# Performance work log

Hardware: AMD Instinct MI355X
Metric: run time of the kernel (lower is better)

The kernel has to match this reference:

```python
import jax, jax.numpy as jnp
import numpy as np

B, C, H, W = 4, 32, 64, 64
D_STATE, D_CONV = 16, 4


def _mamba(x, Win, convw, convb, Wx, Wdt, dtb, Alog, D, Wout, dt_rank):
    Bsz, L, _ = x.shape
    d_in, K = convw.shape
    xz = x @ Win.T                                  # (B, L, 2*d_inner)
    xc, z = xz[..., :d_in], xz[..., d_in:]
    xp = jnp.pad(xc, ((0, 0), (K - 1, 0), (0, 0)))  # causal left pad
    xconv = convb + sum(convw[:, k] * xp[:, k:k + L, :] for k in range(K))
    xa = jax.nn.silu(xconv)                         # (B, L, d_inner)
    xdbl = xa @ Wx.T                                # (B, L, dt_rank + 2*N)
    dt = jax.nn.softplus(xdbl[..., :dt_rank] @ Wdt.T + dtb)     # (B, L, d_inner)
    Bm = xdbl[..., dt_rank:dt_rank + D_STATE]                   # (B, L, N)
    Cm = xdbl[..., dt_rank + D_STATE:]                          # (B, L, N)
    A = -jnp.exp(Alog)                                          # (d_inner, N)
    dA = jnp.exp(dt[..., None] * A)                             # (B, L, d_inner, N)
    dBu = dt[..., None] * Bm[:, :, None, :] * xa[..., None]     # (B, L, d_inner, N)

    def step(h, inp):
        dA_t, dBu_t, C_t = inp
        h = dA_t * h + dBu_t
        return h, jnp.einsum('bdn,bn->bd', h, C_t)

    h0 = jnp.zeros((Bsz, d_in, D_STATE), x.dtype)
    _, ys = jax.lax.scan(step, h0, (dA.transpose(1, 0, 2, 3), dBu.transpose(1, 0, 2, 3), Cm.transpose(1, 0, 2)))
    y = ys.transpose(1, 0, 2) + D * xa
    return (y * jax.nn.silu(z)) @ Wout.T


def _line_seqs(x):
    # x: (B,C,H,W) -> four (B, H*W, C) directional scan orders
    hf = x.reshape(B, C, H * W).transpose(0, 2, 1)
    hb = hf[:, ::-1, :]
    wf = x.transpose(0, 1, 3, 2).reshape(B, C, H * W).transpose(0, 2, 1)
    wb = wf[:, ::-1, :]
    return hf, hb, wf, wb


def _oss(fo1, fo2, p1, p2):
    hf, hb, wf, wb = _line_seqs(fo1)
    fop = jnp.concatenate([hf, hb, wf, wb], axis=2)       # (B, HW, 4C)
    fop = _mamba(fop, *p1, dt_rank=8)
    fop = fop.reshape(B, H * W, 4, C).sum(2)              # (B, HW, C)
    fop = fop.transpose(0, 2, 1).reshape(B, C, H, W)
    residual = fop * fo2
    foc = residual.mean(axis=(2, 3)).reshape(B, C, 1)     # adaptive_avg_pool2d (1,1)
    foc = jnp.concatenate([foc, foc[:, ::-1, :]], axis=2) # (B, C, 2)
    foc = _mamba(foc, *p2, dt_rank=1)
    foc = foc.sum(2, keepdims=True)[..., None]            # (B, C, 1, 1)
    return foc * residual + residual


def setup_inputs() -> dict:
    key = jax.random.key(0)
    ks = jax.random.split(key, 18)
    def n(k, shape, s=0.02):
        return jax.random.normal(k, shape, jnp.float32) * s
    dm1, di1, dr1 = 4 * C, 8 * C, 8
    dm2, di2, dr2 = 2, 4, 1
    return {
        'fo1': jax.random.normal(ks[0], (B, C, H, W), jnp.float32),
        'fo2': jax.random.normal(ks[1], (B, C, H, W), jnp.float32),
        'm1_Win': n(ks[2], (2 * di1, dm1)),
        'm1_convw': n(ks[3], (di1, D_CONV), 0.2),
        'm1_convb': n(ks[4], (di1,), 0.1),
        'm1_Wx': n(ks[5], (dr1 + 2 * D_STATE, di1)),
        'm1_Wdt': n(ks[6], (di1, dr1), 0.1),
        'm1_dtb': n(ks[7], (di1,), 0.5),
        'm1_Alog': jnp.log(jnp.tile(jnp.arange(1, D_STATE + 1, dtype=jnp.float32), (di1, 1))),
        'm1_D': jnp.ones((di1,), jnp.float32),
        'm1_Wout': n(ks[8], (dm1, di1)),
        'm2_Win': n(ks[9], (2 * di2, dm2)),
        'm2_convw': n(ks[10], (di2, D_CONV), 0.2),
        'm2_convb': n(ks[11], (di2,), 0.1),
        'm2_Wx': n(ks[12], (dr2 + 2 * D_STATE, di2)),
        'm2_Wdt': n(ks[13], (di2, dr2), 0.1),
        'm2_dtb': n(ks[14], (di2,), 0.5),
        'm2_Alog': jnp.log(jnp.tile(jnp.arange(1, D_STATE + 1, dtype=jnp.float32), (di2, 1))),
        'm2_D': jnp.ones((di2,), jnp.float32),
        'm2_Wout': n(ks[15], (dm2, di2)),
    }


def reference(fo1, fo2, m1_Win, m1_convw, m1_convb, m1_Wx, m1_Wdt, m1_dtb, m1_Alog, m1_D, m1_Wout,
              m2_Win, m2_convw, m2_convb, m2_Wx, m2_Wdt, m2_dtb, m2_Alog, m2_D, m2_Wout):
    p1 = (m1_Win, m1_convw, m1_convb, m1_Wx, m1_Wdt, m1_dtb, m1_Alog, m1_D, m1_Wout)
    p2 = (m2_Win, m2_convw, m2_convb, m2_Wx, m2_Wdt, m2_dtb, m2_Alog, m2_D, m2_Wout)
    return _oss(fo1, fo2, p1, p2)
```

## Files before the change

kernel.cpp:

```cpp
#include <hip/hip_runtime.h>
#include <cstddef>


typedef __attribute__((ext_vector_type(8))) short short8v;
typedef __attribute__((ext_vector_type(4))) float f32x4;

__device__ __forceinline__ float siluf(float x) { return x / (1.f + __expf(-x)); }
__device__ __forceinline__ float softplusf(float x) { return (x > 20.f) ? x : log1pf(__expf(x)); }
__device__ __forceinline__ unsigned short f2bf(float f) {
  union { float f; unsigned int u; } v; v.f = f;
  unsigned int r = v.u + 0x7fff + ((v.u >> 16) & 1);
  return (unsigned short)(r >> 16);
}
__device__ __forceinline__ float bf2f(unsigned short u) {
  union { unsigned int i; float f; } v; v.i = ((unsigned int)u) << 16; return v.f;
}

__global__ __launch_bounds__(256) void k_build_fop(const float* __restrict__ fo1,
                                                   unsigned short* __restrict__ fopb) {
  int idx = blockIdx.x * 256 + threadIdx.x;
  int j = idx & 127;
  int l = (idx >> 7) & 4095;
  int b = idx >> 19;
  int g = j >> 5, c = j & 31;
  const float* base = fo1 + (size_t)(b * 32 + c) * 4096;
  int li;
  if (g == 0)      li = l;
  else if (g == 1) li = 4095 - l;
  else if (g == 2) li = ((l & 63) << 6) + (l >> 6);
  else { int i2 = 4095 - l; li = ((i2 & 63) << 6) + (i2 >> 6); }
  fopb[idx] = f2bf(base[li]);
}

__global__ __launch_bounds__(256) void k_gemm1_mfma(const unsigned short* __restrict__ A,
                                                    const float* __restrict__ Win,
                                                    unsigned short* __restrict__ xcb,
                                                    float* __restrict__ zbuf) {
  __shared__ unsigned short As[128][136];
  __shared__ unsigned short Bs[64][136];
  int t = threadIdx.x;
  int bm = blockIdx.x * 128, bn = blockIdx.y * 64;
#pragma unroll
  for (int it = 0; it < 8; ++it) {
    int idx = t + it * 256;
    int r = idx >> 4, kc = idx & 15;
    short8v v = *(const short8v*)&A[(size_t)(bm + r) * 128 + kc * 8];
    *(short8v*)&As[r][kc * 8] = v;
  }
#pragma unroll
  for (int it = 0; it < 8; ++it) {
    int idx = t + it * 256;
    int r = idx >> 5, kq = idx & 31;
    float4 w = *(const float4*)&Win[(size_t)(bn + r) * 128 + kq * 4];
    ushort4 h;
    h.x = f2bf(w.x); h.y = f2bf(w.y); h.z = f2bf(w.z); h.w = f2bf(w.w);
    *(ushort4*)&Bs[r][kq * 4] = h;
  }
  __syncthreads();
  int lane = t & 63, w = t >> 6;
  int wm = (w & 1) * 64, wn = (w >> 1) * 32;
  int lr = lane & 15, lg = lane >> 4;
  f32x4 acc[4][2] = {};
#pragma unroll
  for (int k0 = 0; k0 < 128; k0 += 32) {
    short8v a[4], b[2];
#pragma unroll
    for (int mf = 0; mf < 4; ++mf)
      a[mf] = *(const short8v*)&As[wm + mf * 16 + lr][k0 + lg * 8];
#pragma unroll
    for (int nf = 0; nf < 2; ++nf)
      b[nf] = *(const short8v*)&Bs[wn + nf * 16 + lr][k0 + lg * 8];
#pragma unroll
    for (int mf = 0; mf < 4; ++mf)
#pragma unroll
      for (int nf = 0; nf < 2; ++nf)
        acc[mf][nf] = __builtin_amdgcn_mfma_f32_16x16x32_bf16(a[mf], b[nf], acc[mf][nf], 0, 0, 0);
  }
  if (bn < 256) {
#pragma unroll
    for (int mf = 0; mf < 4; ++mf)
#pragma unroll
      for (int nf = 0; nf < 2; ++nf)
#pragma unroll
        for (int r = 0; r < 4; ++r) {
          size_t row = bm + wm + mf * 16 + lg * 4 + r;
          xcb[row * 256 + bn + wn + nf * 16 + lr] = f2bf(acc[mf][nf][r]);
        }
  } else {
#pragma unroll
    for (int mf = 0; mf < 4; ++mf)
#pragma unroll
      for (int nf = 0; nf < 2; ++nf)
#pragma unroll
        for (int r = 0; r < 4; ++r) {
          size_t row = bm + wm + mf * 16 + lg * 4 + r;
          zbuf[row * 256 + (bn - 256) + wn + nf * 16 + lr] = acc[mf][nf][r];
        }
  }
}

__global__ __launch_bounds__(256) void k_gemm_nt(const float* __restrict__ A,
                                                 const float* __restrict__ W,
                                                 float* __restrict__ C,
                                                 int M, int N, int K, int lda) {
  __shared__ float As[32][68];
  __shared__ float Ws[32][68];
  int tid = threadIdx.x;
  int bm = blockIdx.x * 64;
  int bn = blockIdx.y * 64;
  int tx = tid & 15, ty = tid >> 4;
  float acc[4][4] = {};
  for (int k0 = 0; k0 < K; k0 += 32) {
#pragma unroll
    for (int it = 0; it < 2; ++it) {
      int idx = tid + it * 256;
      int r = idx >> 3;
      int kq = idx & 7;
      float4 v = *(const float4*)&A[(size_t)(bm + r) * lda + k0 + kq * 4];
      As[kq * 4 + 0][r] = v.x; As[kq * 4 + 1][r] = v.y;
      As[kq * 4 + 2][r] = v.z; As[kq * 4 + 3][r] = v.w;
      int n = bn + r;
      float4 w = make_float4(0.f, 0.f, 0.f, 0.f);
      if (n < N) w = *(const float4*)&W[(size_t)n * K + k0 + kq * 4];
      Ws[kq * 4 + 0][r] = w.x; Ws[kq * 4 + 1][r] = w.y;
      Ws[kq * 4 + 2][r] = w.z; Ws[kq * 4 + 3][r] = w.w;
    }
    __syncthreads();
#pragma unroll
    for (int k = 0; k < 32; ++k) {
      float4 a = *(const float4*)&As[k][ty * 4];
      float4 w = *(const float4*)&Ws[k][tx * 4];
      float av[4] = {a.x, a.y, a.z, a.w};
      float wv[4] = {w.x, w.y, w.z, w.w};
#pragma unroll
      for (int i = 0; i < 4; ++i)
#pragma unroll
        for (int j = 0; j < 4; ++j)
          acc[i][j] = fmaf(av[i], wv[j], acc[i][j]);
    }
    __syncthreads();
  }
#pragma unroll
  for (int i = 0; i < 4; ++i) {
    size_t m = bm + ty * 4 + i;
#pragma unroll
    for (int j = 0; j < 4; ++j) {
      int n = bn + tx * 4 + j;
      if (n < N) C[m * N + n] = acc[i][j];
    }
  }
}

__global__ __launch_bounds__(256) void k_conv_silu(const unsigned short* __restrict__ xcb,
                                                   const float* __restrict__ convw,
                                                   const float* __restrict__ convb,
                                                   float* __restrict__ xa) {
  int row = blockIdx.x;
  int l = row & 4095;
  int d = threadIdx.x;
  float4 w = *(const float4*)&convw[d * 4];
  float acc = convb[d];
  const unsigned short* p = xcb + (size_t)row * 256 + d;
  if (l >= 3) acc = fmaf(w.x, bf2f(p[-3 * 256]), acc);
  if (l >= 2) acc = fmaf(w.y, bf2f(p[-2 * 256]), acc);
  if (l >= 1) acc = fmaf(w.z, bf2f(p[-1 * 256]), acc);
  acc = fmaf(w.w, bf2f(p[0]), acc);
  xa[(size_t)row * 256 + d] = siluf(acc);
}

__global__ __launch_bounds__(256) void k_scan_p1(const float* __restrict__ xa,
                                                 const float* __restrict__ xdbl,
                                                 const float* __restrict__ Wdt,
                                                 const float* __restrict__ dtb,
                                                 const float* __restrict__ Alog,
                                                 float* __restrict__ Pb,
                                                 float* __restrict__ Qb) {
  __shared__ f32x4 xrow[32][10];
  __shared__ float xas[32][256];
  int t = threadIdx.x;
  int blk = blockIdx.x;
  int ch = blk & 127, b = blk >> 7;
  size_t row0 = (size_t)b * 4096 + ch * 32;
  for (int i = t; i < 320; i += 256) {
    int s = i / 10, q = i - s * 10;
    xrow[s][q] = *(const f32x4*)&xdbl[(row0 + s) * 40 + q * 4];
  }
#pragma unroll
  for (int it = 0; it < 8; ++it) {
    int i = t + it * 256;
    int s = i >> 6, q = i & 63;
    *(f32x4*)&xas[s][q * 4] = *(const f32x4*)&xa[(row0 + s) * 256 + q * 4];
  }
  __syncthreads();
  int d = t;
  f32x4 w0 = *(const f32x4*)&Wdt[d * 8];
  f32x4 w1 = *(const f32x4*)&Wdt[d * 8 + 4];
  float bias = dtb[d];
  float A[16], P[16], Q[16];
#pragma unroll
  for (int g = 0; g < 4; ++g) {
    f32x4 al = *(const f32x4*)&Alog[d * 16 + g * 4];
#pragma unroll
    for (int j = 0; j < 4; ++j) {
      A[g * 4 + j] = -__expf(al[j]);
      P[g * 4 + j] = 1.f;
      Q[g * 4 + j] = 0.f;
    }
  }
#pragma unroll 2
  for (int s = 0; s < 32; ++s) {
    f32x4 x0 = xrow[s][0], x1 = xrow[s][1];
    float v = bias;
#pragma unroll
    for (int j = 0; j < 4; ++j) v = fmaf(x0[j], w0[j], v);
#pragma unroll
    for (int j = 0; j < 4; ++j) v = fmaf(x1[j], w1[j], v);
    float ex = __expf(v);
    float dtv = (v > 20.f) ? v : __logf(1.f + ex);
    float du = dtv * xas[s][d];
    f32x4 bm[4];
#pragma unroll
    for (int g = 0; g < 4; ++g) bm[g] = xrow[s][2 + g];
#pragma unroll
    for (int n = 0; n < 16; ++n) {
      float e = __expf(dtv * A[n]);
      Q[n] = fmaf(e, Q[n], du * bm[n >> 2][n & 3]);
      P[n] *= e;
    }
  }
  size_t ob = (size_t)ch * 16384 + b * 4096 + d * 16;
#pragma unroll
  for (int g = 0; g < 4; ++g) {
    *(f32x4*)&Pb[ob + g * 4] = *(f32x4*)&P[g * 4];
    *(f32x4*)&Qb[ob + g * 4] = *(f32x4*)&Q[g * 4];
  }
}

__global__ __launch_bounds__(256) void k_scan_p2(const float* __restrict__ Pb,
                                                 const float* __restrict__ Qb,
                                                 float* __restrict__ Hin) {
  int t = blockIdx.x * 256 + threadIdx.x;
  float h = 0.f;
  size_t o = t;
#pragma unroll 8
  for (int ch = 0; ch < 128; ++ch) {
    Hin[o] = h;
    h = fmaf(Pb[o], h, Qb[o]);
    o += 16384;
  }
}

__global__ __launch_bounds__(256) void k_scan_p3(const float* __restrict__ xa,
                                                 const float* __restrict__ xdbl,
                                                 const float* __restrict__ Wdt,
                                                 const float* __restrict__ dtb,
                                                 const float* __restrict__ Alog,
                                                 const float* __restrict__ Hin,
                                                 const float* __restrict__ Dp,
                                                 const float* __restrict__ zbuf,
                                                 unsigned short* __restrict__ ym) {
  __shared__ f32x4 xrow[32][10];
  __shared__ float xas[32][256];
  int t = threadIdx.x;
  int blk = blockIdx.x;
  int ch = blk & 127, b = blk >> 7;
  size_t row0 = (size_t)b * 4096 + ch * 32;
  for (int i = t; i < 320; i += 256) {
    int s = i / 10, q = i - s * 10;
    xrow[s][q] = *(const f32x4*)&xdbl[(row0 + s) * 40 + q * 4];
  }
#pragma unroll
  for (int it = 0; it < 8; ++it) {
    int i = t + it * 256;
    int s = i >> 6, q = i & 63;
    *(f32x4*)&xas[s][q * 4] = *(const f32x4*)&xa[(row0 + s) * 256 + q * 4];
  }
  __syncthreads();
  int d = t;
  f32x4 w0 = *(const f32x4*)&Wdt[d * 8];
  f32x4 w1 = *(const f32x4*)&Wdt[d * 8 + 4];
  float bias = dtb[d];
  float Dd = Dp[d];
  float A[16], h[16];
  size_t hb = (size_t)ch * 16384 + b * 4096 + d * 16;
#pragma unroll
  for (int g = 0; g < 4; ++g) {
    f32x4 al = *(const f32x4*)&Alog[d * 16 + g * 4];
    f32x4 hv = *(const f32x4*)&Hin[hb + g * 4];
#pragma unroll
    for (int j = 0; j < 4; ++j) {
      A[g * 4 + j] = -__expf(al[j]);
      h[g * 4 + j] = hv[j];
    }
  }
  const float* zp = zbuf + row0 * 256 + d;
  unsigned short* yo = ym + row0 * 256 + d;
#pragma unroll 2
  for (int s = 0; s < 32; ++s) {
    f32x4 x0 = xrow[s][0], x1 = xrow[s][1];
    float v = bias;
#pragma unroll
    for (int j = 0; j < 4; ++j) v = fmaf(x0[j], w0[j], v);
#pragma unroll
    for (int j = 0; j < 4; ++j) v = fmaf(x1[j], w1[j], v);
    float ex = __expf(v);
    float dtv = (v > 20.f) ? v : __logf(1.f + ex);
    float xav = xas[s][d];
    float du = dtv * xav;
    f32x4 bm[4], cm[4];
#pragma unroll
    for (int g = 0; g < 4; ++g) { bm[g] = xrow[s][2 + g]; cm[g] = xrow[s][6 + g]; }
    float y0 = 0.f, y1 = 0.f, y2 = 0.f, y3 = 0.f;
#pragma unroll
    for (int n = 0; n < 16; n += 4) {
      float e0 = __expf(dtv * A[n]);
      float e1 = __expf(dtv * A[n + 1]);
      float e2 = __expf(dtv * A[n + 2]);
      float e3 = __expf(dtv * A[n + 3]);
      f32x4 bv = bm[n >> 2], cv = cm[n >> 2];
      h[n]     = fmaf(e0, h[n],     du * bv[0]);
      h[n + 1] = fmaf(e1, h[n + 1], du * bv[1]);
      h[n + 2] = fmaf(e2, h[n + 2], du * bv[2]);
      h[n + 3] = fmaf(e3, h[n + 3], du * bv[3]);
      y0 = fmaf(h[n], cv[0], y0);
      y1 = fmaf(h[n + 1], cv[1], y1);
      y2 = fmaf(h[n + 2], cv[2], y2);
      y3 = fmaf(h[n + 3], cv[3], y3);
    }
    float y = (y0 + y1) + (y2 + y3) + Dd * xav;
    float z = zp[s * 256];
    yo[s * 256] = f2bf(y * siluf(z));
  }
}

__global__ __launch_bounds__(256) void k_gemm3res(const unsigned short* __restrict__ ym,
                                                  const float* __restrict__ Wout,
                                                  const float* __restrict__ fo2,
                                                  float* __restrict__ res,
                                                  float* __restrict__ focp) {
  __shared__ unsigned short As[64][264];
  __shared__ unsigned short Bs[32][264];
  __shared__ float fred[4][32];
  int t = threadIdx.x;
  int bm = blockIdx.x * 64;
#pragma unroll
  for (int it = 0; it < 8; ++it) {
    int idx = t + it * 256;
    int r = idx >> 5, kc = idx & 31;
    *(short8v*)&As[r][kc * 8] = *(const short8v*)&ym[(size_t)(bm + r) * 256 + kc * 8];
  }
#pragma unroll
  for (int it = 0; it < 32; ++it) {
    int idx = t + it * 256;
    int n = idx >> 8, k = idx & 255;
    float wv = Wout[(size_t)n * 256 + k] + Wout[(size_t)(n + 32) * 256 + k] +
               Wout[(size_t)(n + 64) * 256 + k] + Wout[(size_t)(n + 96) * 256 + k];
    Bs[n][k] = f2bf(wv);
  }
  __syncthreads();
  int lane = t & 63, w = t >> 6;
  int lr = lane & 15, lg = lane >> 4;
  f32x4 acc0 = {}, acc1 = {};
#pragma unroll
  for (int k0 = 0; k0 < 256; k0 += 32) {
    short8v a  = *(const short8v*)&As[w * 16 + lr][k0 + lg * 8];
    short8v b0 = *(const short8v*)&Bs[lr][k0 + lg * 8];
    short8v b1 = *(const short8v*)&Bs[16 + lr][k0 + lg * 8];
    acc0 = __builtin_amdgcn_mfma_f32_16x16x32_bf16(a, b0, acc0, 0, 0, 0);
    acc1 = __builtin_amdgcn_mfma_f32_16x16x32_bf16(a, b1, acc1, 0, 0, 0);
  }
  int b = bm >> 12;
  float ps0 = 0.f, ps1 = 0.f;
#pragma unroll
  for (int r = 0; r < 4; ++r) {
    int l = (bm + w * 16 + lg * 4 + r) & 4095;
    size_t ri0 = ((size_t)(b * 32 + lr)) * 4096 + l;
    size_t ri1 = ((size_t)(b * 32 + 16 + lr)) * 4096 + l;
    float v0 = acc0[r] * fo2[ri0];
    float v1 = acc1[r] * fo2[ri1];
    res[ri0] = v0; ps0 += v0;
    res[ri1] = v1; ps1 += v1;
  }
  ps0 += __shfl_xor(ps0, 16); ps0 += __shfl_xor(ps0, 32);
  ps1 += __shfl_xor(ps1, 16); ps1 += __shfl_xor(ps1, 32);
  if (lane < 16) { fred[w][lane] = ps0; fred[w][16 + lane] = ps1; }
  __syncthreads();
  if (t < 32)
    focp[((size_t)(b * 32 + t)) * 64 + (blockIdx.x & 63)] =
        fred[0][t] + fred[1][t] + fred[2][t] + fred[3][t];
}

__global__ __launch_bounds__(256) void k_mamba2(const float* __restrict__ focp,
                                                const float* __restrict__ Win2,
                                                const float* __restrict__ convw2,
                                                const float* __restrict__ convb2,
                                                const float* __restrict__ Wx2,
                                                const float* __restrict__ Wdt2,
                                                const float* __restrict__ dtb2,
                                                const float* __restrict__ Alog2,
                                                const float* __restrict__ D2,
                                                const float* __restrict__ Wout2,
                                                float* __restrict__ scale) {
  __shared__ float foc_s[128];
  __shared__ float xz2_s[4][32][8];
  __shared__ float xa2_s[4][32][4];
  __shared__ float xdbl2_s[4][32][33];
  __shared__ float dt2_s[4][32][4];
  __shared__ float ym2_s[4][32][4];
  int t = threadIdx.x;
  if (t < 128) {
    float s = 0.f;
    for (int k = 0; k < 64; ++k) s += focp[(size_t)t * 64 + k];
    foc_s[t] = s * (1.f / 4096.f);
  }
  __syncthreads();
  for (int i = t; i < 1024; i += 256) {
    int j = i & 7, l = (i >> 3) & 31, b = i >> 8;
    float x0 = foc_s[b * 32 + l], x1 = foc_s[b * 32 + 31 - l];
    xz2_s[b][l][j] = x0 * Win2[j * 2] + x1 * Win2[j * 2 + 1];
  }
  __syncthreads();
  for (int i = t; i < 512; i += 256) {
    int d = i & 3, l = (i >> 2) & 31, b = i >> 7;
    float acc = convb2[d];
#pragma unroll
    for (int k = 0; k < 4; ++k) {
      int ls = l + k - 3;
      if (ls >= 0) acc = fmaf(convw2[d * 4 + k], xz2_s[b][ls][d], acc);
    }
    xa2_s[b][l][d] = siluf(acc);
  }
  __syncthreads();
  for (int i = t; i < 4224; i += 256) {
    int r = i % 33, l = (i / 33) & 31, b = i / 1056;
    float s = 0.f;
#pragma unroll
    for (int d = 0; d < 4; ++d) s = fmaf(xa2_s[b][l][d], Wx2[r * 4 + d], s);
    xdbl2_s[b][l][r] = s;
  }
  __syncthreads();
  for (int i = t; i < 512; i += 256) {
    int d = i & 3, l = (i >> 2) & 31, b = i >> 7;
    float s = xdbl2_s[b][l][0] * Wdt2[d] + dtb2[d];
    dt2_s[b][l][d] = softplusf(s);
  }
  __syncthreads();
  {
    int n = t & 15, d = (t >> 4) & 3, b = t >> 6;
    float A = -__expf(Alog2[d * 16 + n]);
    float h = 0.f;
    for (int l = 0; l < 32; ++l) {
      float dtv = dt2_s[b][l][d];
      float xav = xa2_s[b][l][d];
      float e = __expf(dtv * A);
      h = fmaf(e, h, dtv * xdbl2_s[b][l][1 + n] * xav);
      float yp = h * xdbl2_s[b][l][17 + n];
      yp += __shfl_xor(yp, 1);
      yp += __shfl_xor(yp, 2);
      yp += __shfl_xor(yp, 4);
      yp += __shfl_xor(yp, 8);
      if (n == 0) {
        float z = xz2_s[b][l][4 + d];
        float y = yp + D2[d] * xav;
        ym2_s[b][l][d] = y * siluf(z);
      }
    }
  }
  __syncthreads();
  if (t < 128) {
    int l = t & 31, b = t >> 5;
    float s = 0.f;
#pragma unroll
    for (int d = 0; d < 4; ++d) s = fmaf(ym2_s[b][l][d], Wout2[d] + Wout2[4 + d], s);
    scale[t] = s;
  }
}

__global__ __launch_bounds__(256) void k_final(const float* __restrict__ res,
                                               const float* __restrict__ scale,
                                               float* __restrict__ out) {
  int idx = blockIdx.x * 256 + threadIdx.x;
  out[idx] = res[idx] * (1.f + scale[idx >> 12]);
}

extern "C" void kernel_launch(void* const* d_in, const int* in_sizes, int n_in,
                              void* d_out, int out_size, void* d_ws, size_t ws_size,
                              hipStream_t stream) {
  const float* fo1    = (const float*)d_in[0];
  const float* fo2    = (const float*)d_in[1];
  const float* Win    = (const float*)d_in[2];
  const float* convw  = (const float*)d_in[3];
  const float* convb  = (const float*)d_in[4];
  const float* Wx     = (const float*)d_in[5];
  const float* Wdt    = (const float*)d_in[6];
  const float* dtb    = (const float*)d_in[7];
  const float* Alog   = (const float*)d_in[8];
  const float* Dp     = (const float*)d_in[9];
  const float* Wout   = (const float*)d_in[10];
  const float* Win2   = (const float*)d_in[11];
  const float* convw2 = (const float*)d_in[12];
  const float* convb2 = (const float*)d_in[13];
  const float* Wx2    = (const float*)d_in[14];
  const float* Wdt2   = (const float*)d_in[15];
  const float* dtb2   = (const float*)d_in[16];
  const float* Alog2  = (const float*)d_in[17];
  const float* D2     = (const float*)d_in[18];
  const float* Wout2  = (const float*)d_in[19];

  float* ws = (float*)d_ws;
  unsigned short* fopb = (unsigned short*)ws;
  float* xdbl = ws;
  unsigned short* xcb = (unsigned short*)(ws + 1048576);
  float* zbuf = ws + 3145728;
  float* xa   = ws + 7340032;
  float* Pb   = ws + 11534336;
  float* Qb   = ws + 13631488;
  float* Hin  = ws + 15728640;
  unsigned short* ym = (unsigned short*)(ws + 17825792);
  float* res  = ws + 19922944;
  float* focp = ws + 20447232;
  float* scl  = ws + 20455424;
  if (ws_size < (size_t)20455552 * sizeof(float)) return;

  hipLaunchKernelGGL(k_build_fop, dim3(8192), dim3(256), 0, stream, fo1, fopb);
  hipLaunchKernelGGL(k_gemm1_mfma, dim3(128, 8), dim3(256), 0, stream, fopb, Win, xcb, zbuf);
  hipLaunchKernelGGL(k_conv_silu, dim3(16384), dim3(256), 0, stream, xcb, convw, convb, xa);
  hipLaunchKernelGGL(k_gemm_nt, dim3(256, 1), dim3(256), 0, stream,
                     xa, Wx, xdbl, 16384, 40, 256, 256);
  hipLaunchKernelGGL(k_scan_p1, dim3(512), dim3(256), 0, stream,
                     xa, xdbl, Wdt, dtb, Alog, Pb, Qb);
  hipLaunchKernelGGL(k_scan_p2, dim3(64), dim3(256), 0, stream, Pb, Qb, Hin);
  hipLaunchKernelGGL(k_scan_p3, dim3(512), dim3(256), 0, stream,
                     xa, xdbl, Wdt, dtb, Alog, Hin, Dp, zbuf, ym);
  hipLaunchKernelGGL(k_gemm3res, dim3(256), dim3(256), 0, stream, ym, Wout, fo2, res, focp);
  hipLaunchKernelGGL(k_mamba2, dim3(1), dim3(256), 0, stream, focp, Win2, convw2, convb2,
                     Wx2, Wdt2, dtb2, Alog2, D2, Wout2, scl);
  hipLaunchKernelGGL(k_final, dim3(2048), dim3(256), 0, stream, res, scl, (float*)d_out);
}
```

Before: 138.8 us.

## Fuse causal conv+SiLU into x_proj GEMM and store z and xa as bf16

Removes the standalone conv+SiLU kernel. The x_proj GEMM now computes the causal depthwise conv and SiLU on the fly from a haloed tile of xcb in shared memory, and writes xa out as bf16 for the scan kernels. The z half of the input projection is also stored as bf16 instead of fp32. Together these cut one launch and roughly halve the traffic on the xa and z intermediates. In exchange the scans read lower-precision activations, and the fused GEMM still runs on only 256 blocks.

After: 134.8 us. -2.9%, faster.

```diff
diff --git a/kernel.cpp b/kernel.cpp
--- a/kernel.cpp
+++ b/kernel.cpp
@@ -35,7 +35,7 @@
 __global__ __launch_bounds__(256) void k_gemm1_mfma(const unsigned short* __restrict__ A,
                                                     const float* __restrict__ Win,
                                                     unsigned short* __restrict__ xcb,
-                                                    float* __restrict__ zbuf) {
+                                                    unsigned short* __restrict__ zb) {
   __shared__ unsigned short As[128][136];
   __shared__ unsigned short Bs[64][136];
   int t = threadIdx.x;
@@ -76,54 +76,68 @@
       for (int nf = 0; nf < 2; ++nf)
         acc[mf][nf] = __builtin_amdgcn_mfma_f32_16x16x32_bf16(a[mf], b[nf], acc[mf][nf], 0, 0, 0);
   }
-  if (bn < 256) {
-#pragma unroll
-    for (int mf = 0; mf < 4; ++mf)
-#pragma unroll
-      for (int nf = 0; nf < 2; ++nf)
-#pragma unroll
-        for (int r = 0; r < 4; ++r) {
-          size_t row = bm + wm + mf * 16 + lg * 4 + r;
-          xcb[row * 256 + bn + wn + nf * 16 + lr] = f2bf(acc[mf][nf][r]);
-        }
-  } else {
-#pragma unroll
-    for (int mf = 0; mf < 4; ++mf)
-#pragma unroll
-      for (int nf = 0; nf < 2; ++nf)
-#pragma unroll
-        for (int r = 0; r < 4; ++r) {
-          size_t row = bm + wm + mf * 16 + lg * 4 + r;
-          zbuf[row * 256 + (bn - 256) + wn + nf * 16 + lr] = acc[mf][nf][r];
-        }
-  }
-}
-
-__global__ __launch_bounds__(256) void k_gemm_nt(const float* __restrict__ A,
-                                                 const float* __restrict__ W,
-                                                 float* __restrict__ C,
-                                                 int M, int N, int K, int lda) {
+  unsigned short* dst = (bn < 256) ? xcb : zb;
+  int cb = (bn < 256) ? bn : (bn - 256);
+#pragma unroll
+  for (int mf = 0; mf < 4; ++mf)
+#pragma unroll
+    for (int nf = 0; nf < 2; ++nf)
+#pragma unroll
+      for (int r = 0; r < 4; ++r) {
+        size_t row = bm + wm + mf * 16 + lg * 4 + r;
+        dst[row * 256 + cb + wn + nf * 16 + lr] = f2bf(acc[mf][nf][r]);
+      }
+}
+
+__global__ __launch_bounds__(256) void k_gemm2conv(const unsigned short* __restrict__ xcb,
+                                                   const float* __restrict__ convw,
+                                                   const float* __restrict__ convb,
+                                                   const float* __restrict__ Wx,
+                                                   unsigned short* __restrict__ xab,
+                                                   float* __restrict__ xdbl) {
+  __shared__ unsigned short xh[67][36];
   __shared__ float As[32][68];
   __shared__ float Ws[32][68];
-  int tid = threadIdx.x;
+  int t = threadIdx.x;
   int bm = blockIdx.x * 64;
-  int bn = blockIdx.y * 64;
-  int tx = tid & 15, ty = tid >> 4;
+  int b = bm >> 12, lloc0 = bm & 4095;
+  int tx = t & 15, ty = t >> 4;
+  int cc_conv = t & 31;
   float acc[4][4] = {};
-  for (int k0 = 0; k0 < K; k0 += 32) {
+  for (int k0 = 0; k0 < 256; k0 += 32) {
+    for (int i = t; i < 1072; i += 256) {
+      int rr = i >> 4, cc = i & 15;
+      int lloc = lloc0 - 3 + rr;
+      unsigned int val = 0;
+      if (lloc >= 0)
+        val = *(const unsigned int*)&xcb[((size_t)(b * 4096 + lloc)) * 256 + k0 + cc * 2];
+      *(unsigned int*)&xh[rr][cc * 2] = val;
+    }
 #pragma unroll
     for (int it = 0; it < 2; ++it) {
-      int idx = tid + it * 256;
-      int r = idx >> 3;
-      int kq = idx & 7;
-      float4 v = *(const float4*)&A[(size_t)(bm + r) * lda + k0 + kq * 4];
-      As[kq * 4 + 0][r] = v.x; As[kq * 4 + 1][r] = v.y;
-      As[kq * 4 + 2][r] = v.z; As[kq * 4 + 3][r] = v.w;
-      int n = bn + r;
+      int idx = t + it * 256;
+      int r = idx >> 3, kq = idx & 7;
       float4 w = make_float4(0.f, 0.f, 0.f, 0.f);
-      if (n < N) w = *(const float4*)&W[(size_t)n * K + k0 + kq * 4];
+      if (r < 40) w = *(const float4*)&Wx[(size_t)r * 256 + k0 + kq * 4];
       Ws[kq * 4 + 0][r] = w.x; Ws[kq * 4 + 1][r] = w.y;
       Ws[kq * 4 + 2][r] = w.z; Ws[kq * 4 + 3][r] = w.w;
+    }
+    __syncthreads();
+    {
+      float4 w = *(const float4*)&convw[(k0 + cc_conv) * 4];
+      float bias = convb[k0 + cc_conv];
+#pragma unroll
+      for (int it = 0; it < 8; ++it) {
+        int r = (t >> 5) + it * 8;
+        float a = bias;
+        a = fmaf(w.x, bf2f(xh[r][cc_conv]), a);
+        a = fmaf(w.y, bf2f(xh[r + 1][cc_conv]), a);
+        a = fmaf(w.z, bf2f(xh[r + 2][cc_conv]), a);
+        a = fmaf(w.w, bf2f(xh[r + 3][cc_conv]), a);
+        float v = siluf(a);
+        As[cc_conv][r] = v;
+        xab[(size_t)(bm + r) * 256 + k0 + cc_conv] = f2bf(v);
+      }
     }
     __syncthreads();
 #pragma unroll
@@ -145,30 +159,13 @@
     size_t m = bm + ty * 4 + i;
 #pragma unroll
     for (int j = 0; j < 4; ++j) {
-      int n = bn + tx * 4 + j;
-      if (n < N) C[m * N + n] = acc[i][j];
-    }
-  }
-}
-
-__global__ __launch_bounds__(256) void k_conv_silu(const unsigned short* __restrict__ xcb,
-                                                   const float* __restrict__ convw,
-                                                   const float* __restrict__ convb,
-                                                   float* __restrict__ xa) {
-  int row = blockIdx.x;
-  int l = row & 4095;
-  int d = threadIdx.x;
-  float4 w = *(const float4*)&convw[d * 4];
-  float acc = convb[d];
-  const unsigned short* p = xcb + (size_t)row * 256 + d;
-  if (l >= 3) acc = fmaf(w.x, bf2f(p[-3 * 256]), acc);
-  if (l >= 2) acc = fmaf(w.y, bf2f(p[-2 * 256]), acc);
-  if (l >= 1) acc = fmaf(w.z, bf2f(p[-1 * 256]), acc);
-  acc = fmaf(w.w, bf2f(p[0]), acc);
-  xa[(size_t)row * 256 + d] = siluf(acc);
-}
-
-__global__ __launch_bounds__(256) void k_scan_p1(const float* __restrict__ xa,
+      int n = tx * 4 + j;
+      if (n < 40) xdbl[m * 40 + n] = acc[i][j];
+    }
+  }
+}
+
+__global__ __launch_bounds__(256) void k_scan_p1(const unsigned short* __restrict__ xab,
                                                  const float* __restrict__ xdbl,
                                                  const float* __restrict__ Wdt,
                                                  const float* __restrict__ dtb,
@@ -186,10 +183,12 @@
     xrow[s][q] = *(const f32x4*)&xdbl[(row0 + s) * 40 + q * 4];
   }
 #pragma unroll
-  for (int it = 0; it < 8; ++it) {
+  for (int it = 0; it < 4; ++it) {
     int i = t + it * 256;
-    int s = i >> 6, q = i & 63;
-    *(f32x4*)&xas[s][q * 4] = *(const f32x4*)&xa[(row0 + s) * 256 + q * 4];
+    int s = i >> 5, q = i & 31;
+    short8v v = *(const short8v*)&xab[(row0 + s) * 256 + q * 8];
+#pragma unroll
+    for (int j = 0; j < 8; ++j) xas[s][q * 8 + j] = bf2f((unsigned short)v[j]);
   }
   __syncthreads();
   int d = t;
@@ -250,14 +249,14 @@
   }
 }
 
-__global__ __launch_bounds__(256) void k_scan_p3(const float* __restrict__ xa,
+__global__ __launch_bounds__(256) void k_scan_p3(const unsigned short* __restrict__ xab,
                                                  const float* __restrict__ xdbl,
                                                  const float* __restrict__ Wdt,
                                                  const float* __restrict__ dtb,
                                                  const float* __restrict__ Alog,
                                                  const float* __restrict__ Hin,
                                                  const float* __restrict__ Dp,
-                                                 const float* __restrict__ zbuf,
+                                                 const unsigned short* __restrict__ zb,
                                                  unsigned short* __restrict__ ym) {
   __shared__ f32x4 xrow[32][10];
   __shared__ float xas[32][256];
@@ -270,10 +269,12 @@
     xrow[s][q] = *(const f32x4*)&xdbl[(row0 + s) * 40 + q * 4];
   }
 #pragma unroll
-  for (int it = 0; it < 8; ++it) {
+  for (int it = 0; it < 4; ++it) {
     int i = t + it * 256;
-    int s = i >> 6, q = i & 63;
-    *(f32x4*)&xas[s][q * 4] = *(const f32x4*)&xa[(row0 + s) * 256 + q * 4];
+    int s = i >> 5, q = i & 31;
+    short8v v = *(const short8v*)&xab[(row0 + s) * 256 + q * 8];
+#pragma unroll
+    for (int j = 0; j < 8; ++j) xas[s][q * 8 + j] = bf2f((unsigned short)v[j]);
   }
   __syncthreads();
   int d = t;
@@ -293,7 +294,7 @@
       h[g * 4 + j] = hv[j];
     }
   }
-  const float* zp = zbuf + row0 * 256 + d;
+  const unsigned short* zp = zb + row0 * 256 + d;
   unsigned short* yo = ym + row0 * 256 + d;
 #pragma unroll 2
   for (int s = 0; s < 32; ++s) {
@@ -328,7 +329,7 @@
       y3 = fmaf(h[n + 3], cv[3], y3);
     }
     float y = (y0 + y1) + (y2 + y3) + Dd * xav;
-    float z = zp[s * 256];
+    float z = bf2f(zp[s * 256]);
     yo[s * 256] = f2bf(y * siluf(z));
   }
 }
@@ -511,27 +512,26 @@
   unsigned short* fopb = (unsigned short*)ws;
   float* xdbl = ws;
   unsigned short* xcb = (unsigned short*)(ws + 1048576);
-  float* zbuf = ws + 3145728;
-  float* xa   = ws + 7340032;
-  float* Pb   = ws + 11534336;
-  float* Qb   = ws + 13631488;
-  float* Hin  = ws + 15728640;
-  unsigned short* ym = (unsigned short*)(ws + 17825792);
-  float* res  = ws + 19922944;
-  float* focp = ws + 20447232;
-  float* scl  = ws + 20455424;
-  if (ws_size < (size_t)20455552 * sizeof(float)) return;
+  unsigned short* zb  = (unsigned short*)(ws + 3145728);
+  unsigned short* xab = (unsigned short*)(ws + 5242880);
+  float* Pb   = ws + 7340032;
+  float* Qb   = ws + 9437184;
+  float* Hin  = ws + 11534336;
+  unsigned short* ym = (unsigned short*)(ws + 13631488);
+  float* res  = ws + 15728640;
+  float* focp = ws + 16252928;
+  float* scl  = ws + 16261120;
+  if (ws_size < (size_t)16261248 * sizeof(float)) return;
 
   hipLaunchKernelGGL(k_build_fop, dim3(8192), dim3(256), 0, stream, fo1, fopb);
-  hipLaunchKernelGGL(k_gemm1_mfma, dim3(128, 8), dim3(256), 0, stream, fopb, Win, xcb, zbuf);
-  hipLaunchKernelGGL(k_conv_silu, dim3(16384), dim3(256), 0, stream, xcb, convw, convb, xa);
-  hipLaunchKernelGGL(k_gemm_nt, dim3(256, 1), dim3(256), 0, stream,
-                     xa, Wx, xdbl, 16384, 40, 256, 256);
+  hipLaunchKernelGGL(k_gemm1_mfma, dim3(128, 8), dim3(256), 0, stream, fopb, Win, xcb, zb);
+  hipLaunchKernelGGL(k_gemm2conv, dim3(256), dim3(256), 0, stream,
+                     xcb, convw, convb, Wx, xab, xdbl);
   hipLaunchKernelGGL(k_scan_p1, dim3(512), dim3(256), 0, stream,
-                     xa, xdbl, Wdt, dtb, Alog, Pb, Qb);
+                     xab, xdbl, Wdt, dtb, Alog, Pb, Qb);
   hipLaunchKernelGGL(k_scan_p2, dim3(64), dim3(256), 0, stream, Pb, Qb, Hin);
   hipLaunchKernelGGL(k_scan_p3, dim3(512), dim3(256), 0, stream,
-                     xa, xdbl, Wdt, dtb, Alog, Hin, Dp, zbuf, ym);
+                     xab, xdbl, Wdt, dtb, Alog, Hin, Dp, zb, ym);
   hipLaunchKernelGGL(k_gemm3res, dim3(256), dim3(256), 0, stream, ym, Wout, fo2, res, focp);
   hipLaunchKernelGGL(k_mamba2, dim3(1), dim3(256), 0, stream, focp, Win2, convw2, convb2,
                      Wx2, Wdt2, dtb2, Alog2, D2, Wout2, scl);
```
